# Kernel optimization log

Measured on AMD Instinct MI355X. Metric: run time of the kernel, lower is better.

## Reference

```python
import jax, jax.numpy as jnp
import numpy as np

B, M, D, H = 8, 1024, 512, 8


def setup_inputs() -> dict:
    key = jax.random.key(0)
    ks = jax.random.split(key, 8)
    s = 0.02
    return {
        'x': jax.random.normal(ks[0], (B, M, D), jnp.float32),
        'scale': jnp.ones((M, D), jnp.float32),
        'Wq': jax.random.normal(ks[1], (H, D, D), jnp.float32) * s,
        'Wk': jax.random.normal(ks[2], (H, D, D), jnp.float32) * s,
        'Wv': jax.random.normal(ks[3], (H, D, D), jnp.float32) * s,
        'Wo': jax.random.normal(ks[4], (D, H * D), jnp.float32) * s,
        'bo': jnp.zeros((D,), jnp.float32),
        'Wff': jax.random.normal(ks[5], (D, D), jnp.float32) * s,
        'bff': jnp.zeros((D,), jnp.float32),
        'Wg': jax.random.normal(ks[6], (D, D), jnp.float32) * s,
        'bg': jnp.zeros((D,), jnp.float32),
        'Wl': jax.random.normal(ks[7], (D, D), jnp.float32) * s,
        'bl': jnp.zeros((D,), jnp.float32),
        'beta': jnp.ones((1,), jnp.float32),
    }


def _rope_cos_sin(m, d):
    # theta = 10000 ** (-2*(i-1)/d), faithful to the original (note the i-1 quirk)
    i = jnp.arange(d // 2, dtype=jnp.float32)
    theta = jnp.power(10000.0, -2.0 * (i - 1.0) / d)
    ang = jnp.arange(m, dtype=jnp.float32)[:, None] * theta[None, :]  # [m, d/2]
    return jnp.cos(ang), jnp.sin(ang)


def _apply_rope(t, cos, sin):
    # t: [..., m, d]; equivalent to bmm with the block-diagonal rotation matrix R[p]
    te, to = t[..., 0::2], t[..., 1::2]
    re = te * cos + to * sin
    ro = -te * sin + to * cos
    return jnp.stack([re, ro], axis=-1).reshape(t.shape)


def _rmsnorm(x, scale):
    b, m, d = x.shape
    ff_rms = jnp.sqrt(jnp.sum(x * x, axis=(1, 2))) * (m * d) ** (-0.5)  # [b]
    return scale[None, :m, :] * (x / ff_rms[:, None, None])


def reference(x, scale, Wq, Wk, Wv, Wo, bo, Wff, bff, Wg, bg, Wl, bl, beta):
    b, m, d = x.shape
    xn = _rmsnorm(x, scale)

    # per-head full-width projections (nn.Linear: y = x @ W.T)
    q = jnp.einsum('bmd,hod->hbmo', xn, Wq)  # [H,B,M,D]
    k = jnp.einsum('bmd,hod->hbmo', xn, Wk)
    v = jnp.einsum('bmd,hod->hbmo', xn, Wv)

    cos, sin = _rope_cos_sin(m, d)
    qr = _apply_rope(q, cos, sin)
    kr = _apply_rope(k, cos, sin)

    # SDPA with is_causal=False (no mask); dropout disabled (eval)
    scores = jnp.einsum('hbqd,hbkd->hbqk', qr, kr) / jnp.sqrt(jnp.float32(d))
    attn = jax.nn.softmax(scores, axis=-1)
    ctx = jnp.einsum('hbqk,hbkd->hbqd', attn, v)  # [H,B,M,D]

    cat = jnp.transpose(ctx, (1, 2, 0, 3)).reshape(b, m, -1)  # [B,M,H*D]
    attn_out = cat @ Wo.T + bo

    x2 = xn + attn_out
    x3 = _rmsnorm(x2, scale)

    h1 = x3 @ Wff.T + bff
    g = h1 @ Wg.T + bg
    sw = g * jax.nn.sigmoid(beta * g)
    ff = sw * (h1 @ Wl.T + bl)
    return x3 + ff
```

## Files before the change

kernel.cpp:

```cpp
#include <hip/hip_runtime.h>
#include <math.h>

typedef unsigned short u16;
typedef float f32x4 __attribute__((ext_vector_type(4)));
typedef __bf16 bf16x8 __attribute__((ext_vector_type(8)));
typedef unsigned short u16x8 __attribute__((ext_vector_type(8)));

__device__ __forceinline__ float bf2f(u16 u) {
    union { float f; unsigned int i; } v; v.i = ((unsigned int)u) << 16; return v.f;
}
__device__ __forceinline__ u16 f2bf(float f) {
    union { float f; unsigned int i; } v; v.f = f;
    unsigned int r = v.i + 0x7fffu + ((v.i >> 16) & 1u);
    return (u16)(r >> 16);
}

__device__ __forceinline__ void gll(const u16* g, u16* l) {
    __builtin_amdgcn_global_load_lds((const __attribute__((address_space(1))) void*)g,
                                     (__attribute__((address_space(3))) void*)l, 16, 0, 0);
}

struct EpiBF16 {
    u16* C; long zs; int ldc;
    __device__ void operator()(int z, int m, int n, float v) const {
        C[(long)z * zs + (long)m * ldc + n] = f2bf(v);
    }
};
struct EpiScale {
    u16* C; long zs; int ldc; float s;
    __device__ void operator()(int z, int m, int n, float v) const {
        C[(long)z * zs + (long)m * ldc + n] = f2bf(v * s);
    }
};
struct EpiAcc {
    float* x2;
    __device__ void operator()(int z, int m, int n, float v) const {
        x2[(long)m * 512 + n] += v;
    }
};
struct EpiBias16 {
    u16* C; const float* bias;
    __device__ void operator()(int z, int m, int n, float v) const {
        C[(long)m * 512 + n] = f2bf(v + bias[n]);
    }
};
struct EpiGL {
    u16* g; u16* l; const float* bg; const float* bl;
    __device__ void operator()(int z, int m, int n, float v) const {
        if (n < 512) g[(long)m * 512 + n] = f2bf(v + bg[n]);
        else         l[(long)m * 512 + n - 512] = f2bf(v + bl[n - 512]);
    }
};
struct EpiQKV3 {
    u16* q; u16* k; u16* vT; const float* cosT; const float* sinT;
    __device__ void operator()(int z, int m, int n, float val) const {
        int which = z >> 3, h = z & 7;
        if (which < 2) {
            float pv = __shfl_xor(val, 1, 64);
            int mm = m & 1023, j0 = n >> 1;
            float c = cosT[mm * 256 + j0], s = sinT[mm * 256 + j0];
            float o = (n & 1) ? (val * c - pv * s) : (val * c + pv * s);
            u16* dst = which ? k : q;
            dst[((long)h << 22) + (long)m * 512 + n] = f2bf(o);
        } else {
            vT[((long)h << 22) + ((long)(m >> 10) << 19) + ((long)n << 10) + (m & 1023)] = f2bf(val);
        }
    }
};
struct EpiCtxMul {
    u16* C; const float* rr;
    __device__ void operator()(int z, int m, int n, float v) const {
        C[(long)z * 524288 + (long)m * 512 + n] = f2bf(v * rr[(long)z * 1024 + m]);
    }
};

struct EpiScores {
    u16* C; float* rs; float sscale;
    __device__ float elem(int z, int m, int n, float v) const {
        float e = expf(v * sscale);
        C[(long)z * 1048576 + (long)m * 1024 + n] = f2bf(e);
        return e;
    }
    __device__ void row(int z, int m, float p, int l15) const {
        p += __shfl_xor(p, 1, 64); p += __shfl_xor(p, 2, 64);
        p += __shfl_xor(p, 4, 64); p += __shfl_xor(p, 8, 64);
        if (l15 == 0) atomicAdd(rs + (long)z * 1024 + m, p);
    }
};
struct EpiAccA {
    float* x2;
    __device__ float elem(int z, int m, int n, float v) const {
        atomicAdd(x2 + (long)m * 512 + n, v);
        return 0.f;
    }
    __device__ void row(int, int, float, int) const {}
};

#define RDA(S, I) (*(const bf16x8*)(lds + (S) * 8192 + (I) * 512 + aro))
#define RDB(S, J) (*(const bf16x8*)(lds + (S) * 8192 + (J) * 512 + bro))
#define MFMA_PH(JP) do { \
    __builtin_amdgcn_s_barrier(); \
    asm volatile("s_waitcnt lgkmcnt(0)" ::: "memory"); \
    __builtin_amdgcn_sched_barrier(0); \
    __builtin_amdgcn_s_setprio(1); \
    _Pragma("unroll") \
    for (int i_ = 0; i_ < 8; i_++) { \
        acc[i_][2*(JP)]   = __builtin_amdgcn_mfma_f32_16x16x32_bf16(aF[i_], bF[0], acc[i_][2*(JP)], 0, 0, 0); \
        acc[i_][2*(JP)+1] = __builtin_amdgcn_mfma_f32_16x16x32_bf16(aF[i_], bF[1], acc[i_][2*(JP)+1], 0, 0, 0); \
    } \
    __builtin_amdgcn_s_setprio(0); \
} while (0)

template <class Epi>
__launch_bounds__(512, 2)
__global__ void gemm256(const u16* __restrict__ A, const u16* __restrict__ B,
                        int nkh, int kssh, int lda, int ldb,
                        long aBatch, long bBatch, long aSeg, long bSeg, Epi epi) {
    __shared__ __align__(16) u16 lds[65536];
    const int t = threadIdx.x;
    const int lane = t & 63, wave = t >> 6;
    const int wr = wave >> 2, wc = wave & 3;
    const int l15 = lane & 15, quad = lane >> 4;
    const int m0 = blockIdx.x * 256, n0 = blockIdx.y * 256;
    const int z = blockIdx.z;
    const int sr = t >> 2;
    const int scw = ((t & 3) ^ ((t >> 3) & 3)) * 8;
    const u16* gA = A + (long)z * aBatch + (long)(m0 + sr) * lda + scw;
    const u16* gB = B + (long)z * bBatch + (long)(n0 + sr) * ldb + scw;
    const long a128 = 128L * lda, b128 = 128L * ldb;
    u16* lA0 = lds + wave * 512 + lane * 8;
    u16* lB0 = lds + 32768 + wave * 512 + lane * 8;
    const int kmask = (1 << kssh) - 1;

    auto STA = [&](int shp) {
        int c = shp < nkh ? shp : nkh - 1;
        const u16* s = gA + (long)(c >> kssh) * aSeg + (c & kmask) * 32;
        u16* d = lA0 + (shp & 3) * 8192;
        gll(s, d); gll(s + a128, d + 4096);
    };
    auto STB = [&](int shp) {
        int c = shp < nkh ? shp : nkh - 1;
        const u16* s = gB + (long)(c >> kssh) * bSeg + (c & kmask) * 32;
        u16* d = lB0 + (shp & 3) * 8192;
        gll(s, d); gll(s + b128, d + 4096);
    };

    const int ap = (quad ^ ((l15 >> 1) & 3)) * 8;
    const int aro = (wr * 128 + l15) * 32 + ap;
    const int bro = 32768 + (wc * 64 + l15) * 32 + ap;
    f32x4 acc[8][4] = {};

    STA(0); STB(0); STA(1); STB(1); STA(2); STB(2);
    asm volatile("s_waitcnt vmcnt(4)" ::: "memory");
    __builtin_amdgcn_s_barrier();

    const int niter = nkh >> 2;
    int sh = 3;
    for (int it = 0; it < niter; it++) {
        bf16x8 aF[8], bF[2];
        #pragma unroll
        for (int i = 0; i < 8; i++) aF[i] = RDA(0, i);
        bF[0] = RDB(0, 0); bF[1] = RDB(0, 1);
        STA(sh);
        MFMA_PH(0);
        __builtin_amdgcn_s_barrier();
        bF[0] = RDB(0, 2); bF[1] = RDB(0, 3);
        STB(sh);
        MFMA_PH(1);
        __builtin_amdgcn_s_barrier();
        #pragma unroll
        for (int i = 0; i < 8; i++) aF[i] = RDA(1, i);
        bF[0] = RDB(1, 0); bF[1] = RDB(1, 1);
        STA(sh + 1);
        MFMA_PH(0);
        __builtin_amdgcn_s_barrier();
        bF[0] = RDB(1, 2); bF[1] = RDB(1, 3);
        STB(sh + 1);
        MFMA_PH(1);
        asm volatile("s_waitcnt vmcnt(4)" ::: "memory");
        __builtin_amdgcn_s_barrier();
        #pragma unroll
        for (int i = 0; i < 8; i++) aF[i] = RDA(2, i);
        bF[0] = RDB(2, 0); bF[1] = RDB(2, 1);
        STA(sh + 2);
        MFMA_PH(0);
        __builtin_amdgcn_s_barrier();
        bF[0] = RDB(2, 2); bF[1] = RDB(2, 3);
        STB(sh + 2);
        MFMA_PH(1);
        __builtin_amdgcn_s_barrier();
        #pragma unroll
        for (int i = 0; i < 8; i++) aF[i] = RDA(3, i);
        bF[0] = RDB(3, 0); bF[1] = RDB(3, 1);
        STA(sh + 3);
        MFMA_PH(0);
        __builtin_amdgcn_s_barrier();
        bF[0] = RDB(3, 2); bF[1] = RDB(3, 3);
        STB(sh + 3);
        MFMA_PH(1);
        asm volatile("s_waitcnt vmcnt(4)" ::: "memory");
        __builtin_amdgcn_s_barrier();
        sh += 4;
    }
    asm volatile("s_waitcnt vmcnt(0)" ::: "memory");

    #pragma unroll
    for (int i = 0; i < 8; i++)
        #pragma unroll
        for (int r = 0; r < 4; r++) {
            int m = m0 + wr * 128 + i * 16 + quad * 4 + r;
            float p = 0.f;
            #pragma unroll
            for (int j = 0; j < 4; j++)
                p += epi.elem(z, m, n0 + wc * 64 + j * 16 + l15, acc[i][j][r]);
            epi.row(z, m, p, l15);
        }
}
#undef RDA
#undef RDB
#undef MFMA_PH

template <class Epi>
__launch_bounds__(256, 4)
__global__ void gemm128(const u16* __restrict__ A, const u16* __restrict__ B,
                        int Kseg, int nSeg, int lda, int ldb,
                        long aBatch, long bBatch, long aSeg, Epi epi) {
    __shared__ __align__(16) u16 sA[8192];
    __shared__ __align__(16) u16 sB[8192];
    const int t = threadIdx.x;
    const int lane = t & 63, wave = t >> 6;
    const int wr = wave >> 1, wc = wave & 1;
    const int l15 = lane & 15, quad = lane >> 4;
    const int m0 = blockIdx.x * 128, n0 = blockIdx.y * 128;
    const int sr = t >> 2;
    const int scw = ((t & 3) ^ ((t >> 3) & 3)) * 8;
    const u16* gA = A + (long)blockIdx.z * aBatch + (long)(m0 + sr) * lda + scw;
    const u16* gB = B + (long)blockIdx.z * bBatch + (long)(n0 + sr) * ldb + scw;
    const long a2 = 64L * lda, b2 = 64L * ldb;
    u16* lA = sA + wave * 512 + lane * 8;
    u16* lB = sB + wave * 512 + lane * 8;
    const int ap = (quad ^ ((l15 >> 1) & 3)) * 8;
    const int ab = (wr * 64 + l15) * 32 + ap;
    const int bb = (wc * 64 + l15) * 32 + ap;
    f32x4 acc[4][4] = {};
    for (int s = 0; s < nSeg; s++) {
        const u16* gAs = gA + (long)s * aSeg;
        const u16* gBs = gB + s * Kseg;
        for (int k0 = 0; k0 < Kseg; k0 += 64) {
            gll(gAs + k0, lA);             gll(gAs + k0 + a2, lA + 2048);
            gll(gBs + k0, lB);             gll(gBs + k0 + b2, lB + 2048);
            gll(gAs + k0 + 32, lA + 4096); gll(gAs + k0 + 32 + a2, lA + 6144);
            gll(gBs + k0 + 32, lB + 4096); gll(gBs + k0 + 32 + b2, lB + 6144);
            __syncthreads();
            #pragma unroll
            for (int half = 0; half < 2; half++) {
                bf16x8 aF[4], bF[4];
                #pragma unroll
                for (int i = 0; i < 4; i++) aF[i] = *(const bf16x8*)(sA + half * 4096 + ab + i * 512);
                #pragma unroll
                for (int j = 0; j < 4; j++) bF[j] = *(const bf16x8*)(sB + half * 4096 + bb + j * 512);
                #pragma unroll
                for (int i = 0; i < 4; i++)
                    #pragma unroll
                    for (int j = 0; j < 4; j++)
                        acc[i][j] = __builtin_amdgcn_mfma_f32_16x16x32_bf16(aF[i], bF[j], acc[i][j], 0, 0, 0);
            }
            __syncthreads();
        }
    }
    #pragma unroll
    for (int i = 0; i < 4; i++)
        #pragma unroll
        for (int j = 0; j < 4; j++)
            #pragma unroll
            for (int r = 0; r < 4; r++)
                epi(blockIdx.z, m0 + wr * 64 + i * 16 + quad * 4 + r,
                    n0 + wc * 64 + j * 16 + l15, acc[i][j][r]);
}

__device__ __forceinline__ float waveSum(float v) {
    #pragma unroll
    for (int o = 32; o > 0; o >>= 1) v += __shfl_down(v, o, 64);
    return v;
}

__global__ void sumsq_f32(const float* __restrict__ x, float* __restrict__ part) {
    __shared__ float tmp[4];
    long base = (long)blockIdx.x * 524288 + (long)blockIdx.y * 8192;
    float s = 0.f;
    for (int i = threadIdx.x; i < 8192; i += 256) { float v = x[base + i]; s += v * v; }
    s = waveSum(s);
    if ((threadIdx.x & 63) == 0) tmp[threadIdx.x >> 6] = s;
    __syncthreads();
    if (threadIdx.x == 0) part[blockIdx.x * 64 + blockIdx.y] = tmp[0] + tmp[1] + tmp[2] + tmp[3];
}
__global__ void finalize_inv(const float* __restrict__ part, float* __restrict__ inv) {
    float s = part[blockIdx.x * 64 + threadIdx.x];
    s = waveSum(s);
    if (threadIdx.x == 0) inv[blockIdx.x] = sqrtf(524288.0f / s);
}
__global__ void rmsnorm1f(const float* __restrict__ x, const float* __restrict__ scale,
                          const float* __restrict__ inv, const float* __restrict__ bo,
                          u16* __restrict__ xnb, float* __restrict__ x2) {
    long i = (long)blockIdx.x * 256 + threadIdx.x;
    int b = (int)(i >> 19), md = (int)(i & 524287);
    float v = x[i] * inv[b] * scale[md];
    xnb[i] = f2bf(v);
    x2[i] = v + bo[i & 511];
}
__global__ void rmsnorm2(const float* __restrict__ x2, const float* __restrict__ scale,
                         const float* __restrict__ inv, u16* __restrict__ x3b) {
    long i = (long)blockIdx.x * 256 + threadIdx.x;
    int b = (int)(i >> 19), md = (int)(i & 524287);
    x3b[i] = f2bf(x2[i] * inv[b] * scale[md]);
}
__global__ void rope_tables(float* __restrict__ cosT, float* __restrict__ sinT) {
    int i = blockIdx.x * 256 + threadIdx.x;
    int m = i >> 8, j = i & 255;
    float theta = powf(10000.0f, -2.0f * ((float)j - 1.0f) / 512.0f);
    float ang = (float)m * theta;
    cosT[i] = cosf(ang); sinT[i] = sinf(ang);
}
__global__ void rope_apply(u16* __restrict__ tq, const float* __restrict__ cosT,
                           const float* __restrict__ sinT) {
    long i = (long)blockIdx.x * 256 + threadIdx.x;
    int j = (int)(i & 255), m = (int)((i >> 8) & 1023);
    float c = cosT[m * 256 + j], s = sinT[m * 256 + j];
    long base = i * 2;
    float te = bf2f(tq[base]), to = bf2f(tq[base + 1]);
    tq[base]     = f2bf(te * c + to * s);
    tq[base + 1] = f2bf(-te * s + to * c);
}
__global__ void transpose_v(const u16* __restrict__ v, u16* __restrict__ vT) {
    __shared__ u16 tile[32][33];
    long zb = (long)blockIdx.z * 524288;
    int mo = blockIdx.x * 32, oo = blockIdx.y * 32;
    int tx = threadIdx.x & 31, ty = threadIdx.x >> 5;
    for (int r = ty; r < 32; r += 8) tile[r][tx] = v[zb + (long)(mo + r) * 512 + oo + tx];
    __syncthreads();
    for (int r = ty; r < 32; r += 8) vT[zb + (long)(oo + r) * 1024 + mo + tx] = tile[tx][r];
}
__launch_bounds__(256)
__global__ void softmax_rows4(u16* __restrict__ sc) {
    int row = blockIdx.x * 4 + (threadIdx.x >> 6);
    int lane = threadIdx.x & 63;
    u16* p = sc + (long)row * 1024 + lane * 16;
    float v[16]; float mx = -1e30f;
    #pragma unroll
    for (int i = 0; i < 16; i++) { v[i] = bf2f(p[i]); mx = fmaxf(mx, v[i]); }
    #pragma unroll
    for (int o = 32; o > 0; o >>= 1) mx = fmaxf(mx, __shfl_xor(mx, o, 64));
    float s = 0.f;
    #pragma unroll
    for (int i = 0; i < 16; i++) { v[i] = expf(v[i] - mx); s += v[i]; }
    #pragma unroll
    for (int o = 32; o > 0; o >>= 1) s += __shfl_xor(s, o, 64);
    float r = 1.0f / s;
    #pragma unroll
    for (int i = 0; i < 16; i++) p[i] = f2bf(v[i] * r);
}
__global__ void final_out(const float* __restrict__ x2, const float* __restrict__ scale,
                          const float* __restrict__ inv2, const u16* __restrict__ g,
                          const u16* __restrict__ l, const float* __restrict__ beta,
                          float* __restrict__ out) {
    long i = (long)blockIdx.x * 256 + threadIdx.x;
    int b = (int)(i >> 19), md = (int)(i & 524287);
    float x3 = x2[i] * inv2[b] * scale[md];
    float gv = bf2f(g[i]), lv = bf2f(l[i]);
    float bta = beta[0];
    float sw = gv / (1.0f + expf(-bta * gv));
    out[i] = x3 + sw * lv;
}
__global__ void convert_f2b(const float* __restrict__ s, u16* __restrict__ d, int n) {
    int i = blockIdx.x * 256 + threadIdx.x;
    if (i < n) d[i] = f2bf(s[i]);
}
__global__ void convert3(const float* __restrict__ a, const float* __restrict__ b,
                         const float* __restrict__ c, u16* __restrict__ d) {
    int i = blockIdx.x * 256 + threadIdx.x;
    const float* s = (i < 262144) ? a : (i < 524288) ? b : c;
    d[i] = f2bf(s[i & 262143]);
}
__global__ void zero_f32(float* __restrict__ p) {
    p[blockIdx.x * 256 + threadIdx.x] = 0.f;
}
__global__ void recip_f32(float* __restrict__ p) {
    int i = blockIdx.x * 256 + threadIdx.x;
    p[i] = 1.0f / p[i];
}

#define MB 1048576L
extern "C" void kernel_launch(void* const* d_in, const int* in_sizes, int n_in,
                              void* d_out, int out_size, void* d_ws, size_t ws_size,
                              hipStream_t stream) {
    (void)in_sizes; (void)n_in; (void)out_size;
    const float* x    = (const float*)d_in[0];
    const float* scale= (const float*)d_in[1];
    const float* Wq   = (const float*)d_in[2];
    const float* Wk   = (const float*)d_in[3];
    const float* Wv   = (const float*)d_in[4];
    const float* Wo   = (const float*)d_in[5];
    const float* bo   = (const float*)d_in[6];
    const float* Wff  = (const float*)d_in[7];
    const float* bff  = (const float*)d_in[8];
    const float* Wg   = (const float*)d_in[9];
    const float* bg   = (const float*)d_in[10];
    const float* Wl   = (const float*)d_in[11];
    const float* bl   = (const float*)d_in[12];
    const float* beta = (const float*)d_in[13];
    float* out = (float*)d_out;
    char* ws = (char*)d_ws;
    const float sscale = 0.044194173824159216f;

    if (ws_size >= 260000000UL) {
        u16*   xnb   = (u16*)  (ws);
        u16*   q_all = (u16*)  (ws + 8*MB);
        u16*   k_all = (u16*)  (ws + 72*MB);
        u16*   vT_all= (u16*)  (ws + 136*MB);
        u16*   sc    = (u16*)  (ws + 200*MB);
        u16*   Wqkvb = (u16*)  (ws + 200*MB);
        u16*   Wob   = (u16*)  (ws + 232*MB);
        u16*   Wffb  = (u16*)  (ws + 236*MB);
        u16*   Wglb  = (u16*)  (ws + 236*MB + 524288L);
        float* cosT  = (float*)(ws + 237*MB + 1572864L);
        float* sinT  = (float*)(ws + 238*MB + 1572864L);
        float* rowsum= (float*)(ws + 239*MB + 1572864L);
        float* part  = (float*)(ws + 239*MB + 1835008L);
        float* inv1  = part + 512;
        float* inv2  = part + 528;
        float* x2    = out;
        u16* x3b = k_all; u16* h1 = k_all + 4194304; u16* g = k_all + 8388608; u16* l = k_all + 12582912;

        sumsq_f32<<<dim3(8, 64), 256, 0, stream>>>(x, part);
        finalize_inv<<<8, 64, 0, stream>>>(part, inv1);
        rmsnorm1f<<<16384, 256, 0, stream>>>(x, scale, inv1, bo, xnb, x2);
        rope_tables<<<1024, 256, 0, stream>>>(cosT, sinT);
        zero_f32<<<256, 256, 0, stream>>>(rowsum);
        convert_f2b<<<8192, 256, 0, stream>>>(Wq, Wqkvb, 2097152);
        convert_f2b<<<8192, 256, 0, stream>>>(Wk, Wqkvb + 2097152, 2097152);
        convert_f2b<<<8192, 256, 0, stream>>>(Wv, Wqkvb + 4194304, 2097152);
        convert_f2b<<<8192, 256, 0, stream>>>(Wo, Wob, 2097152);
        convert_f2b<<<1024, 256, 0, stream>>>(Wff, Wffb, 262144);
        convert_f2b<<<1024, 256, 0, stream>>>(Wg, Wglb, 262144);
        convert_f2b<<<1024, 256, 0, stream>>>(Wl, Wglb + 262144, 262144);

        gemm128<<<dim3(64, 4, 24), 256, 0, stream>>>(xnb, Wqkvb, 512, 1, 512, 512,
            0L, 262144L, 0L, EpiQKV3{q_all, k_all, vT_all, cosT, sinT});

        for (int h0 = 0; h0 < 8; h0 += 2) {
            const long off = (long)h0 * 4194304;
            float* rsc = rowsum + (long)h0 * 8192;
            gemm256<<<dim3(4, 4, 16), 512, 0, stream>>>(q_all + off, k_all + off, 16, 4, 512, 512,
                524288L, 524288L, 512L, 512L, EpiScores{sc, rsc, sscale});
            recip_f32<<<64, 256, 0, stream>>>(rsc);
            gemm128<<<dim3(8, 4, 16), 256, 0, stream>>>(sc, vT_all + off, 1024, 1, 1024, 1024,
                1048576L, 524288L, 0L, EpiCtxMul{q_all + off, rsc});
        }
        gemm256<<<dim3(32, 2, 4), 512, 0, stream>>>(q_all, Wob, 32, 4, 512, 4096,
            8388608L, 1024L, 4194304L, 512L, EpiAccA{x2});

        sumsq_f32<<<dim3(8, 64), 256, 0, stream>>>(x2, part);
        finalize_inv<<<8, 64, 0, stream>>>(part, inv2);
        rmsnorm2<<<16384, 256, 0, stream>>>(x2, scale, inv2, x3b);

        gemm128<<<dim3(64, 4, 1), 256, 0, stream>>>(x3b, Wffb, 512, 1, 512, 512,
            0L, 0L, 0L, EpiBias16{h1, bff});
        gemm128<<<dim3(64, 8, 1), 256, 0, stream>>>(h1, Wglb, 512, 1, 512, 512,
            0L, 0L, 0L, EpiGL{g, l, bg, bl});
        final_out<<<16384, 256, 0, stream>>>(x2, scale, inv2, g, l, beta, out);
        return;
    }

    u16*   xnb  = (u16*)  (ws);
    float* x2   = (float*)(ws + 8388608L);
    u16*   qh   = (u16*)  (ws + 25165824L);
    u16*   kh   = (u16*)  (ws + 33554432L);
    u16*   vhc  = (u16*)  (ws + 41943040L);
    u16*   vT   = (u16*)  (ws + 50331648L);
    u16*   Whb  = (u16*)  (ws + 58720256L);
    u16*   Wob  = (u16*)  (ws + 60293120L);
    u16*   Wfb  = (u16*)  (ws + 64487424L);
    u16*   Wgb  = (u16*)  (ws + 65011712L);
    u16*   Wlb  = (u16*)  (ws + 65536000L);
    float* cosT = (float*)(ws + 66060288L);
    float* sinT = (float*)(ws + 67108864L);
    float* part = (float*)(ws + 68157440L);
    float* inv1 = (float*)(ws + 68159488L);
    float* inv2 = (float*)(ws + 68159552L);
    u16*   sc   = (u16*)  (ws + 68159616L);
    u16*   x3b = qh;  u16* h1 = kh;  u16* g = vhc;  u16* l = vT;
    const bool big = ws_size >= 85002240UL;

    sumsq_f32<<<dim3(8, 64), 256, 0, stream>>>(x, part);
    finalize_inv<<<8, 64, 0, stream>>>(part, inv1);
    rmsnorm1f<<<16384, 256, 0, stream>>>(x, scale, inv1, bo, xnb, x2);
    rope_tables<<<1024, 256, 0, stream>>>(cosT, sinT);
    convert_f2b<<<8192, 256, 0, stream>>>(Wo, Wob, 2097152);
    convert_f2b<<<1024, 256, 0, stream>>>(Wff, Wfb, 262144);
    convert_f2b<<<1024, 256, 0, stream>>>(Wg, Wgb, 262144);
    convert_f2b<<<1024, 256, 0, stream>>>(Wl, Wlb, 262144);

    for (int h = 0; h < 8; h++) {
        convert3<<<3072, 256, 0, stream>>>(Wq + (long)h * 262144, Wk + (long)h * 262144,
                                           Wv + (long)h * 262144, Whb);
        gemm128<<<dim3(64, 4, 3), 256, 0, stream>>>(xnb, Whb, 512, 1, 512, 512, 0L, 262144L, 0L,
                                                    EpiBF16{qh, 4194304L, 512});
        rope_apply<<<16384, 256, 0, stream>>>(qh, cosT, sinT);
        transpose_v<<<dim3(32, 16, 8), 256, 0, stream>>>(vhc, vT);
        if (big) {
            gemm128<<<dim3(8, 8, 8), 256, 0, stream>>>(qh, kh, 512, 1, 512, 512, 524288L, 524288L,
                                                       0L, EpiScale{sc, 1048576L, 1024, sscale});
            softmax_rows4<<<2048, 256, 0, stream>>>(sc);
            gemm128<<<dim3(8, 4, 8), 256, 0, stream>>>(sc, vT, 1024, 1, 1024, 1024, 1048576L,
                                                       524288L, 0L, EpiBF16{vhc, 524288L, 512});
        } else {
            for (int b = 0; b < 8; b++) {
                gemm128<<<dim3(8, 8, 1), 256, 0, stream>>>(qh + (long)b * 524288, kh + (long)b * 524288,
                                                           512, 1, 512, 512, 0L, 0L, 0L,
                                                           EpiScale{sc, 0L, 1024, sscale});
                softmax_rows4<<<256, 256, 0, stream>>>(sc);
                gemm128<<<dim3(8, 4, 1), 256, 0, stream>>>(sc, vT + (long)b * 524288, 1024, 1, 1024,
                                                           1024, 0L, 0L, 0L,
                                                           EpiBF16{vhc + (long)b * 524288, 0L, 512});
            }
        }
        gemm128<<<dim3(64, 4, 1), 256, 0, stream>>>(vhc, Wob + (long)h * 512, 512, 1, 512, 4096,
                                                    0L, 0L, 0L, EpiAcc{x2});
    }

    sumsq_f32<<<dim3(8, 64), 256, 0, stream>>>(x2, part);
    finalize_inv<<<8, 64, 0, stream>>>(part, inv2);
    rmsnorm2<<<16384, 256, 0, stream>>>(x2, scale, inv2, x3b);
    gemm128<<<dim3(64, 4, 1), 256, 0, stream>>>(x3b, Wfb, 512, 1, 512, 512, 0L, 0L, 0L,
                                                EpiBias16{h1, bff});
    gemm128<<<dim3(64, 4, 1), 256, 0, stream>>>(h1, Wgb, 512, 1, 512, 512, 0L, 0L, 0L,
                                                EpiBias16{g, bg});
    gemm128<<<dim3(64, 4, 1), 256, 0, stream>>>(h1, Wlb, 512, 1, 512, 512, 0L, 0L, 0L,
                                                EpiBias16{l, bl});
    final_out<<<16384, 256, 0, stream>>>(x2, scale, inv2, g, l, beta, out);
}
```

Baseline: 757.1 us.

## Merge prep kernels, fold norm finalize into consumers, move QKV onto gemm256

Merges the seven weight-conversion launches into one vectorized prep kernel. Folds rowsum zeroing into the rope-table kernel, which now writes interleaved cos/sin. The separate finalize_inv and recip launches are dropped: the inverse norm is recomputed per wave from the partial sums, and the reciprocal is taken in the ctx epilogue. The QKV projection moves from gemm128 to two gemm256 launches, with V computed transposed so vT is written contiguously. This cuts launch count and per-launch overhead, at the cost of each thread in the elementwise kernels redundantly reducing 64 partials.

After: 671.5 us. 1.13x faster.

```diff
diff --git a/kernel.cpp b/kernel.cpp
--- a/kernel.cpp
+++ b/kernel.cpp
@@ -51,29 +51,35 @@
         else         l[(long)m * 512 + n - 512] = f2bf(v + bl[n - 512]);
     }
 };
-struct EpiQKV3 {
-    u16* q; u16* k; u16* vT; const float* cosT; const float* sinT;
-    __device__ void operator()(int z, int m, int n, float val) const {
-        int which = z >> 3, h = z & 7;
-        if (which < 2) {
-            float pv = __shfl_xor(val, 1, 64);
-            int mm = m & 1023, j0 = n >> 1;
-            float c = cosT[mm * 256 + j0], s = sinT[mm * 256 + j0];
-            float o = (n & 1) ? (val * c - pv * s) : (val * c + pv * s);
-            u16* dst = which ? k : q;
-            dst[((long)h << 22) + (long)m * 512 + n] = f2bf(o);
-        } else {
-            vT[((long)h << 22) + ((long)(m >> 10) << 19) + ((long)n << 10) + (m & 1023)] = f2bf(val);
-        }
-    }
-};
 struct EpiCtxMul {
-    u16* C; const float* rr;
+    u16* C; const float* rs;
     __device__ void operator()(int z, int m, int n, float v) const {
-        C[(long)z * 524288 + (long)m * 512 + n] = f2bf(v * rr[(long)z * 1024 + m]);
-    }
-};
-
+        float r = __builtin_amdgcn_rcpf(rs[(long)z * 1024 + m]);
+        C[(long)z * 524288 + (long)m * 512 + n] = f2bf(v * r);
+    }
+};
+
+struct EpiQKR {
+    u16* q; u16* k; const float* csT;
+    __device__ float elem(int z, int m, int n, float val) const {
+        float pv = __shfl_xor(val, 1, 64);
+        int mm = m & 1023, j0 = n >> 1;
+        float c = csT[(mm * 256 + j0) * 2], s = csT[(mm * 256 + j0) * 2 + 1];
+        float o = (n & 1) ? (val * c - pv * s) : (val * c + pv * s);
+        u16* dst = (z >> 3) ? k : q;
+        dst[((long)(z & 7) << 22) + (long)m * 512 + n] = f2bf(o);
+        return 0.f;
+    }
+    __device__ void row(int, int, float, int) const {}
+};
+struct EpiVT {
+    u16* vT;
+    __device__ float elem(int z, int m, int n, float v) const {
+        vT[((long)z << 22) + ((long)(n >> 10) << 19) + ((long)m << 10) + (n & 1023)] = f2bf(v);
+        return 0.f;
+    }
+    __device__ void row(int, int, float, int) const {}
+};
 struct EpiScores {
     u16* C; float* rs; float sscale;
     __device__ float elem(int z, int m, int n, float v) const {
@@ -283,6 +289,12 @@
     for (int o = 32; o > 0; o >>= 1) v += __shfl_down(v, o, 64);
     return v;
 }
+__device__ __forceinline__ float invFromPart(const float* part, int b) {
+    float s = part[b * 64 + (threadIdx.x & 63)];
+    s = waveSum(s);
+    s = __shfl(s, 0, 64);
+    return sqrtf(524288.0f / s);
+}
 
 __global__ void sumsq_f32(const float* __restrict__ x, float* __restrict__ part) {
     __shared__ float tmp[4];
@@ -299,6 +311,36 @@
     s = waveSum(s);
     if (threadIdx.x == 0) inv[blockIdx.x] = sqrtf(524288.0f / s);
 }
+__global__ void rmsnorm1f_a(const float* __restrict__ x, const float* __restrict__ scale,
+                            const float* __restrict__ part, const float* __restrict__ bo,
+                            u16* __restrict__ xnb, float* __restrict__ x2) {
+    long i = (long)blockIdx.x * 256 + threadIdx.x;
+    int b = (int)(i >> 19), md = (int)(i & 524287);
+    float inv = invFromPart(part, b);
+    float v = x[i] * inv * scale[md];
+    xnb[i] = f2bf(v);
+    x2[i] = v + bo[i & 511];
+}
+__global__ void rmsnorm2_a(const float* __restrict__ x2, const float* __restrict__ scale,
+                           const float* __restrict__ part, u16* __restrict__ x3b) {
+    long i = (long)blockIdx.x * 256 + threadIdx.x;
+    int b = (int)(i >> 19), md = (int)(i & 524287);
+    float inv = invFromPart(part, b);
+    x3b[i] = f2bf(x2[i] * inv * scale[md]);
+}
+__global__ void final_out_a(const float* __restrict__ x2, const float* __restrict__ scale,
+                            const float* __restrict__ part, const u16* __restrict__ g,
+                            const u16* __restrict__ l, const float* __restrict__ beta,
+                            float* __restrict__ out) {
+    long i = (long)blockIdx.x * 256 + threadIdx.x;
+    int b = (int)(i >> 19), md = (int)(i & 524287);
+    float inv2 = invFromPart(part, b);
+    float x3 = x2[i] * inv2 * scale[md];
+    float gv = bf2f(g[i]), lv = bf2f(l[i]);
+    float bta = beta[0];
+    float sw = gv / (1.0f + expf(-bta * gv));
+    out[i] = x3 + sw * lv;
+}
 __global__ void rmsnorm1f(const float* __restrict__ x, const float* __restrict__ scale,
                           const float* __restrict__ inv, const float* __restrict__ bo,
                           u16* __restrict__ xnb, float* __restrict__ x2) {
@@ -313,6 +355,26 @@
     long i = (long)blockIdx.x * 256 + threadIdx.x;
     int b = (int)(i >> 19), md = (int)(i & 524287);
     x3b[i] = f2bf(x2[i] * inv[b] * scale[md]);
+}
+__global__ void final_out(const float* __restrict__ x2, const float* __restrict__ scale,
+                          const float* __restrict__ inv2, const u16* __restrict__ g,
+                          const u16* __restrict__ l, const float* __restrict__ beta,
+                          float* __restrict__ out) {
+    long i = (long)blockIdx.x * 256 + threadIdx.x;
+    int b = (int)(i >> 19), md = (int)(i & 524287);
+    float x3 = x2[i] * inv2[b] * scale[md];
+    float gv = bf2f(g[i]), lv = bf2f(l[i]);
+    float bta = beta[0];
+    float sw = gv / (1.0f + expf(-bta * gv));
+    out[i] = x3 + sw * lv;
+}
+__global__ void rope_tables_a(float* __restrict__ csT, float* __restrict__ rowsum) {
+    int i = blockIdx.x * 256 + threadIdx.x;
+    int m = i >> 8, j = i & 255;
+    float theta = powf(10000.0f, -2.0f * ((float)j - 1.0f) / 512.0f);
+    float ang = (float)m * theta;
+    csT[2 * i] = cosf(ang); csT[2 * i + 1] = sinf(ang);
+    if (i < 65536) rowsum[i] = 0.f;
 }
 __global__ void rope_tables(float* __restrict__ cosT, float* __restrict__ sinT) {
     int i = blockIdx.x * 256 + threadIdx.x;
@@ -359,17 +421,27 @@
     #pragma unroll
     for (int i = 0; i < 16; i++) p[i] = f2bf(v[i] * r);
 }
-__global__ void final_out(const float* __restrict__ x2, const float* __restrict__ scale,
-                          const float* __restrict__ inv2, const u16* __restrict__ g,
-                          const u16* __restrict__ l, const float* __restrict__ beta,
-                          float* __restrict__ out) {
-    long i = (long)blockIdx.x * 256 + threadIdx.x;
-    int b = (int)(i >> 19), md = (int)(i & 524287);
-    float x3 = x2[i] * inv2[b] * scale[md];
-    float gv = bf2f(g[i]), lv = bf2f(l[i]);
-    float bta = beta[0];
-    float sw = gv / (1.0f + expf(-bta * gv));
-    out[i] = x3 + sw * lv;
+__device__ __forceinline__ void cvt8(const float* __restrict__ s, u16* __restrict__ d) {
+    f32x4 a = *(const f32x4*)s, b = *(const f32x4*)(s + 4);
+    u16x8 o;
+    o[0] = f2bf(a[0]); o[1] = f2bf(a[1]); o[2] = f2bf(a[2]); o[3] = f2bf(a[3]);
+    o[4] = f2bf(b[0]); o[5] = f2bf(b[1]); o[6] = f2bf(b[2]); o[7] = f2bf(b[3]);
+    *(u16x8*)d = o;
+}
+__global__ void prep_w(const float* __restrict__ Wq, const float* __restrict__ Wk,
+                       const float* __restrict__ Wv, const float* __restrict__ Wo,
+                       const float* __restrict__ Wff, const float* __restrict__ Wg,
+                       const float* __restrict__ Wl,
+                       u16* __restrict__ Wqkvb, u16* __restrict__ Wob,
+                       u16* __restrict__ Wffb, u16* __restrict__ Wglb) {
+    long i = ((long)blockIdx.x * 256 + threadIdx.x) * 8;
+    if (i < 2097152)      cvt8(Wq + i, Wqkvb + i);
+    else if (i < 4194304) cvt8(Wk + (i - 2097152), Wqkvb + i);
+    else if (i < 6291456) cvt8(Wv + (i - 4194304), Wqkvb + i);
+    else if (i < 8388608) cvt8(Wo + (i - 6291456), Wob + (i - 6291456));
+    else if (i < 8650752) cvt8(Wff + (i - 8388608), Wffb + (i - 8388608));
+    else if (i < 8912896) cvt8(Wg + (i - 8650752), Wglb + (i - 8650752));
+    else                  cvt8(Wl + (i - 8912896), Wglb + 262144 + (i - 8912896));
 }
 __global__ void convert_f2b(const float* __restrict__ s, u16* __restrict__ d, int n) {
     int i = blockIdx.x * 256 + threadIdx.x;
@@ -380,13 +452,6 @@
     int i = blockIdx.x * 256 + threadIdx.x;
     const float* s = (i < 262144) ? a : (i < 524288) ? b : c;
     d[i] = f2bf(s[i & 262143]);
-}
-__global__ void zero_f32(float* __restrict__ p) {
-    p[blockIdx.x * 256 + threadIdx.x] = 0.f;
-}
-__global__ void recip_f32(float* __restrict__ p) {
-    int i = blockIdx.x * 256 + threadIdx.x;
-    p[i] = 1.0f / p[i];
 }
 
 #define MB 1048576L
@@ -422,37 +487,28 @@
         u16*   Wob   = (u16*)  (ws + 232*MB);
         u16*   Wffb  = (u16*)  (ws + 236*MB);
         u16*   Wglb  = (u16*)  (ws + 236*MB + 524288L);
-        float* cosT  = (float*)(ws + 237*MB + 1572864L);
-        float* sinT  = (float*)(ws + 238*MB + 1572864L);
+        float* csT   = (float*)(ws + 237*MB + 1572864L);
         float* rowsum= (float*)(ws + 239*MB + 1572864L);
         float* part  = (float*)(ws + 239*MB + 1835008L);
-        float* inv1  = part + 512;
-        float* inv2  = part + 528;
         float* x2    = out;
         u16* x3b = k_all; u16* h1 = k_all + 4194304; u16* g = k_all + 8388608; u16* l = k_all + 12582912;
 
         sumsq_f32<<<dim3(8, 64), 256, 0, stream>>>(x, part);
-        finalize_inv<<<8, 64, 0, stream>>>(part, inv1);
-        rmsnorm1f<<<16384, 256, 0, stream>>>(x, scale, inv1, bo, xnb, x2);
-        rope_tables<<<1024, 256, 0, stream>>>(cosT, sinT);
-        zero_f32<<<256, 256, 0, stream>>>(rowsum);
-        convert_f2b<<<8192, 256, 0, stream>>>(Wq, Wqkvb, 2097152);
-        convert_f2b<<<8192, 256, 0, stream>>>(Wk, Wqkvb + 2097152, 2097152);
-        convert_f2b<<<8192, 256, 0, stream>>>(Wv, Wqkvb + 4194304, 2097152);
-        convert_f2b<<<8192, 256, 0, stream>>>(Wo, Wob, 2097152);
-        convert_f2b<<<1024, 256, 0, stream>>>(Wff, Wffb, 262144);
-        convert_f2b<<<1024, 256, 0, stream>>>(Wg, Wglb, 262144);
-        convert_f2b<<<1024, 256, 0, stream>>>(Wl, Wglb + 262144, 262144);
-
-        gemm128<<<dim3(64, 4, 24), 256, 0, stream>>>(xnb, Wqkvb, 512, 1, 512, 512,
-            0L, 262144L, 0L, EpiQKV3{q_all, k_all, vT_all, cosT, sinT});
+        rmsnorm1f_a<<<16384, 256, 0, stream>>>(x, scale, part, bo, xnb, x2);
+        rope_tables_a<<<1024, 256, 0, stream>>>(csT, rowsum);
+        prep_w<<<4480, 256, 0, stream>>>(Wq, Wk, Wv, Wo, Wff, Wg, Wl,
+                                         Wqkvb, Wob, Wffb, Wglb);
+
+        gemm256<<<dim3(32, 2, 16), 512, 0, stream>>>(xnb, Wqkvb, 16, 4, 512, 512,
+            0L, 262144L, 512L, 512L, EpiQKR{q_all, k_all, csT});
+        gemm256<<<dim3(2, 32, 8), 512, 0, stream>>>(Wqkvb + 4194304, xnb, 16, 4, 512, 512,
+            262144L, 0L, 512L, 512L, EpiVT{vT_all});
 
         for (int h0 = 0; h0 < 8; h0 += 2) {
             const long off = (long)h0 * 4194304;
             float* rsc = rowsum + (long)h0 * 8192;
             gemm256<<<dim3(4, 4, 16), 512, 0, stream>>>(q_all + off, k_all + off, 16, 4, 512, 512,
                 524288L, 524288L, 512L, 512L, EpiScores{sc, rsc, sscale});
-            recip_f32<<<64, 256, 0, stream>>>(rsc);
             gemm128<<<dim3(8, 4, 16), 256, 0, stream>>>(sc, vT_all + off, 1024, 1, 1024, 1024,
                 1048576L, 524288L, 0L, EpiCtxMul{q_all + off, rsc});
         }
@@ -460,14 +516,13 @@
             8388608L, 1024L, 4194304L, 512L, EpiAccA{x2});
 
         sumsq_f32<<<dim3(8, 64), 256, 0, stream>>>(x2, part);
-        finalize_inv<<<8, 64, 0, stream>>>(part, inv2);
-        rmsnorm2<<<16384, 256, 0, stream>>>(x2, scale, inv2, x3b);
+        rmsnorm2_a<<<16384, 256, 0, stream>>>(x2, scale, part, x3b);
 
         gemm128<<<dim3(64, 4, 1), 256, 0, stream>>>(x3b, Wffb, 512, 1, 512, 512,
             0L, 0L, 0L, EpiBias16{h1, bff});
         gemm128<<<dim3(64, 8, 1), 256, 0, stream>>>(h1, Wglb, 512, 1, 512, 512,
             0L, 0L, 0L, EpiGL{g, l, bg, bl});
-        final_out<<<16384, 256, 0, stream>>>(x2, scale, inv2, g, l, beta, out);
+        final_out_a<<<16384, 256, 0, stream>>>(x2, scale, part, g, l, beta, out);
         return;
     }
 
```
